# Kernel optimization log

Hardware: AMD Instinct MI355X
Metric: run time of the kernel (lower is better)

The kernel has to match this reference:

```python
import jax, jax.numpy as jnp
import numpy as np

B, T, HID = 16, 512, 1024
NH, NKV, D = 8, 4, 128
THETA = 10000.0


def setup_inputs() -> dict:
    key = jax.random.key(0)
    k0, k1, k2, k3, k4 = jax.random.split(key, 5)
    s = 0.02
    return {
        "hidden_states": jax.random.normal(k0, (B, T, HID), dtype=jnp.float32),
        "Wq": s * jax.random.normal(k1, (HID, NH * D), dtype=jnp.float32),
        "Wk": s * jax.random.normal(k2, (HID, NKV * D), dtype=jnp.float32),
        "Wv": s * jax.random.normal(k3, (HID, NKV * D), dtype=jnp.float32),
        "Wo": s * jax.random.normal(k4, (NH * D, HID), dtype=jnp.float32),
    }


def _rotate_half(x):
    x1, x2 = x[..., : x.shape[-1] // 2], x[..., x.shape[-1] // 2:]
    return jnp.concatenate((-x2, x1), axis=-1)


def reference(hidden_states, Wq, Wk, Wv, Wo):
    b, t, _ = hidden_states.shape
    # projections -> [B, H, T, D]
    q = (hidden_states @ Wq).reshape(b, t, NH, D).transpose(0, 2, 1, 3)
    k = (hidden_states @ Wk).reshape(b, t, NKV, D).transpose(0, 2, 1, 3)
    v = (hidden_states @ Wv).reshape(b, t, NKV, D).transpose(0, 2, 1, 3)

    # RoPE: cos/sin [T, D]
    inv_freq = 1.0 / (THETA ** (jnp.arange(0, D, 2, dtype=jnp.float32) / D))
    freqs = jnp.outer(jnp.arange(t, dtype=jnp.float32), inv_freq)
    emb = jnp.concatenate((freqs, freqs), axis=-1)
    cos, sin = jnp.cos(emb), jnp.sin(emb)
    q = q * cos + _rotate_half(q) * sin
    k = k * cos + _rotate_half(k) * sin

    # repeat_interleave KV heads to match query heads (GQA)
    groups = NH // NKV
    k = jnp.repeat(k, groups, axis=1)  # [B, NH, T, D]
    v = jnp.repeat(v, groups, axis=1)

    scale = 1.0 / jnp.sqrt(jnp.float32(D))
    attn = jnp.einsum("bhtd,bhsd->bhts", q, k) * scale  # [B, NH, T, T]
    causal = jnp.triu(jnp.ones((t, t), dtype=bool), k=1)
    attn = jnp.where(causal, -jnp.inf, attn)
    attn = jax.nn.softmax(attn, axis=-1)  # dropout p=0 (eval)

    out = jnp.einsum("bhts,bhsd->bhtd", attn, v)
    out = out.transpose(0, 2, 1, 3).reshape(b, t, NH * D)
    return out @ Wo  # [B, T, HID]
```

## Files before the change

kernel.cpp:

```cpp
#include <hip/hip_runtime.h>
#include <hip/hip_bf16.h>
#include <math.h>

#define Bn 16
#define Tn 512
#define HIDn 1024
#define NHn 8
#define NKVn 4
#define Dn 128

typedef __attribute__((ext_vector_type(8))) short short8;
typedef __attribute__((ext_vector_type(4))) float floatx4;

__device__ __forceinline__ short bf16r(float f) {
  __hip_bfloat16 h = __float2bfloat16(f);
  return *(short*)&h;
}
__device__ __forceinline__ float bf16f(short s) {
  __hip_bfloat16 h = *(__hip_bfloat16*)&s;
  return __bfloat162float(h);
}

__device__ __forceinline__ void g2l16(const short* g, short* l) {
  __builtin_amdgcn_global_load_lds(
      (const __attribute__((address_space(1))) void*)g,
      (__attribute__((address_space(3))) void*)l, 16, 0, 0);
}

__global__ __launch_bounds__(256) void prep_kernel(const float* __restrict__ X,
                                                   const float* __restrict__ Wq,
                                                   const float* __restrict__ Wk,
                                                   const float* __restrict__ Wv,
                                                   const float* __restrict__ Wo,
                                                   short* __restrict__ Xb,
                                                   short* __restrict__ BtQKV,
                                                   short* __restrict__ Wot) {
  __shared__ float tile[32][33];
  int bid = blockIdx.x;
  if (bid < 4096) {
    int i = bid * 256 + threadIdx.x;
    const float4* p = reinterpret_cast<const float4*>(X) + (size_t)i * 2;
    float4 a = p[0], b = p[1];
    short8 o;
    o[0] = bf16r(a.x); o[1] = bf16r(a.y); o[2] = bf16r(a.z); o[3] = bf16r(a.w);
    o[4] = bf16r(b.x); o[5] = bf16r(b.y); o[6] = bf16r(b.z); o[7] = bf16r(b.w);
    reinterpret_cast<short8*>(Xb)[i] = o;
    return;
  }
  int t = bid - 4096;
  const float* in;
  short* out;
  int N;
  if (t < 1024)      { in = Wq; out = BtQKV;               N = 1024; }
  else if (t < 1536) { t -= 1024; in = Wk; out = BtQKV + 1024 * 1024; N = 512; }
  else if (t < 2048) { t -= 1536; in = Wv; out = BtQKV + 1536 * 1024; N = 512; }
  else               { t -= 2048; in = Wo; out = Wot;                N = 1024; }
  int ntx = N >> 5;
  int n0 = (t % ntx) * 32, k0 = (t / ntx) * 32;
  int tx = threadIdx.x & 31, ty = threadIdx.x >> 5;
  for (int i = 0; i < 32; i += 8)
    tile[ty + i][tx] = in[(size_t)(k0 + ty + i) * N + n0 + tx];
  __syncthreads();
  for (int i = 0; i < 32; i += 8)
    out[(size_t)(n0 + ty + i) * 1024 + k0 + tx] = bf16r(tile[tx][ty + i]);
}

__global__ __launch_bounds__(512, 2) void gemm_qkv(const short* __restrict__ A,
                                                   const short* __restrict__ Bt,
                                                   short* __restrict__ Cqkv,
                                                   short* __restrict__ Vt) {
  __shared__ __align__(16) short SH[65536];
  const int tid = threadIdx.x;
  const int wave = tid >> 6, lane = tid & 63;
  const int quad = lane >> 4, l16 = lane & 15;
  const int wr = wave >> 2, wc = wave & 3;
  int fid = blockIdx.y * 8 + blockIdx.x;
  int swz = (fid & 7) * 32 + (fid >> 3);
  const int bx = swz & 7;
  const int m0 = (swz >> 3) << 8, n0 = bx << 8;
  const int nt = 16;

  floatx4 acc[2][2][4][2];
#pragma unroll
  for (int r = 0; r < 2; ++r)
#pragma unroll
    for (int c = 0; c < 2; ++c)
#pragma unroll
      for (int mi = 0; mi < 4; ++mi)
#pragma unroll
        for (int ni = 0; ni < 2; ++ni)
          acc[r][c][mi][ni] = (floatx4){0.f, 0.f, 0.f, 0.f};

  const int srow = tid >> 3;
  const int schunk = (tid & 7) ^ (srow & 7);

#define STAGE(tile_, src_, row0_, ldso_)                                             \
  do {                                                                               \
    int t_ = (tile_);                                                                \
    if (t_ < nt) {                                                                   \
      short* bb_ = SH + ((t_ & 1) << 15) + (ldso_);                                  \
      const short* sp_ =                                                             \
          (src_) + ((size_t)((row0_) + srow) << 10) + (t_ << 6) + (schunk << 3);     \
      g2l16(sp_, bb_ + (wave << 9));                                                 \
      g2l16(sp_ + (64 << 10), bb_ + 4096 + (wave << 9));                             \
    }                                                                                \
  } while (0)

#define LDA(dst_, rhalf_)                                                            \
  do {                                                                               \
    _Pragma("unroll") for (int mi = 0; mi < 4; ++mi) {                               \
      int R = (rhalf_) * 128 + wr * 64 + mi * 16 + l16;                              \
      _Pragma("unroll") for (int k = 0; k < 2; ++k) {                                \
        int pos = (k * 4 + quad) ^ (R & 7);                                          \
        dst_[mi][k] = *(const short8*)&Ab[R * 64 + pos * 8];                         \
      }                                                                              \
    }                                                                                \
  } while (0)

#define LDB(dst_, chalf_)                                                            \
  do {                                                                               \
    _Pragma("unroll") for (int ni = 0; ni < 2; ++ni) {                               \
      int R = (chalf_) * 128 + wc * 32 + ni * 16 + l16;                              \
      _Pragma("unroll") for (int k = 0; k < 2; ++k) {                                \
        int pos = (k * 4 + quad) ^ (R & 7);                                          \
        dst_[ni][k] = *(const short8*)&Bb[R * 64 + pos * 8];                         \
      }                                                                              \
    }                                                                                \
  } while (0)

#define MFMA_Q(r_, c_, a_, b_)                                                       \
  do {                                                                               \
    _Pragma("unroll") for (int mi = 0; mi < 4; ++mi)                                 \
        _Pragma("unroll") for (int ni = 0; ni < 2; ++ni) {                           \
      acc[r_][c_][mi][ni] = __builtin_amdgcn_mfma_f32_16x16x32_bf16(                 \
          a_[mi][0], b_[ni][0], acc[r_][c_][mi][ni], 0, 0, 0);                       \
      acc[r_][c_][mi][ni] = __builtin_amdgcn_mfma_f32_16x16x32_bf16(                 \
          a_[mi][1], b_[ni][1], acc[r_][c_][mi][ni], 0, 0, 0);                       \
    }                                                                                \
  } while (0)

#define PH_OPEN()                                                                    \
  do {                                                                               \
    __builtin_amdgcn_s_barrier();                                                    \
    __builtin_amdgcn_s_setprio(1);                                                   \
  } while (0)
#define PH_CLOSE()                                                                   \
  do {                                                                               \
    __builtin_amdgcn_s_setprio(0);                                                   \
    __builtin_amdgcn_s_barrier();                                                    \
  } while (0)

  STAGE(0, A, m0, 0);
  STAGE(0, Bt, n0 + 128, 24576);
  STAGE(0, Bt, n0, 16384);
  STAGE(0, A, m0 + 128, 8192);
  STAGE(1, A, m0, 0);
  STAGE(1, Bt, n0 + 128, 24576);
  STAGE(1, Bt, n0, 16384);
  asm volatile("s_waitcnt vmcnt(6)" ::: "memory");
  __builtin_amdgcn_s_barrier();

  short8 afA[4][2], afB[4][2], bf0[2][2], bf1[2][2];
  for (int g = 0; g < nt; ++g) {
    const short* Ab = SH + ((g & 1) << 15);
    const short* Bb = Ab + 16384;
    LDA(afA, 0);
    LDB(bf0, 0);
    LDB(bf1, 1);
    STAGE(g + 1, A, m0 + 128, 8192);
    PH_OPEN();
    MFMA_Q(0, 0, afA, bf0);
    PH_CLOSE();
    LDA(afB, 1);
    STAGE(g + 2, A, m0, 0);
    PH_OPEN();
    MFMA_Q(0, 1, afA, bf1);
    PH_CLOSE();
    STAGE(g + 2, Bt, n0 + 128, 24576);
    PH_OPEN();
    MFMA_Q(1, 1, afB, bf1);
    PH_CLOSE();
    STAGE(g + 2, Bt, n0, 16384);
    PH_OPEN();
    MFMA_Q(1, 0, afB, bf0);
    __builtin_amdgcn_s_setprio(0);
    if (g + 2 < nt)
      asm volatile("s_waitcnt vmcnt(6)" ::: "memory");
    else
      asm volatile("s_waitcnt vmcnt(0)" ::: "memory");
    __builtin_amdgcn_s_barrier();
  }

  if (bx < 6) {
#pragma unroll
    for (int r = 0; r < 2; ++r)
#pragma unroll
      for (int c = 0; c < 2; ++c)
#pragma unroll
        for (int mi = 0; mi < 4; ++mi)
#pragma unroll
          for (int ni = 0; ni < 2; ++ni)
#pragma unroll
            for (int rr = 0; rr < 4; ++rr) {
              int row = m0 + r * 128 + wr * 64 + mi * 16 + quad * 4 + rr;
              int col = n0 + c * 128 + wc * 32 + ni * 16 + l16;
              Cqkv[(size_t)row * 2048 + col] = bf16r(acc[r][c][mi][ni][rr]);
            }
  } else {
    const int b = m0 >> 9, t0 = m0 & (Tn - 1);
#pragma unroll
    for (int ch = 0; ch < 2; ++ch) {
      __syncthreads();
#pragma unroll
      for (int r = 0; r < 2; ++r)
#pragma unroll
        for (int mi = 0; mi < 4; ++mi)
#pragma unroll
          for (int ni = 0; ni < 2; ++ni)
#pragma unroll
            for (int rr = 0; rr < 4; ++rr) {
              int t = r * 128 + wr * 64 + mi * 16 + quad * 4 + rr;
              int d = wc * 32 + ni * 16 + l16;
              SH[d * 264 + t] = bf16r(acc[r][ch][mi][ni][rr]);
            }
      __syncthreads();
      int kv = (bx - 6) * 2 + ch;
#pragma unroll
      for (int u = 0; u < 8; ++u) {
        int idx = tid + u * 512;
        int d = idx >> 5, tb = (idx & 31) << 3;
        short8 vv = *(short8*)&SH[d * 264 + tb];
        *(short8*)&Vt[((size_t)(b * NKVn + kv) * 128 + d) * Tn + t0 + tb] = vv;
      }
    }
  }
#undef STAGE
#undef LDA
#undef LDB
#undef MFMA_Q
#undef PH_OPEN
#undef PH_CLOSE
}

__global__ void rope_k_kernel(short* __restrict__ C) {
  int idx = blockIdx.x * blockDim.x + threadIdx.x;
  int vec = idx & 7;
  int head = (idx >> 3) & 3;
  int bt = idx >> 5;
  int t = bt & (Tn - 1);
  int i0 = vec * 8;
  size_t base = (size_t)bt * 2048 + 1024 + head * 128 + i0;
  short8 x1 = *(short8*)&C[base];
  short8 x2 = *(short8*)&C[base + 64];
  short8 o1, o2;
  float tf = (float)t;
#pragma unroll
  for (int j = 0; j < 8; ++j) {
    float a = tf * exp2f(-0.2076205059f * (float)(i0 + j));
    float s, c;
    sincosf(a, &s, &c);
    float v1 = bf16f(x1[j]), v2 = bf16f(x2[j]);
    o1[j] = bf16r(v1 * c - v2 * s);
    o2[j] = bf16r(v2 * c + v1 * s);
  }
  *(short8*)&C[base] = o1;
  *(short8*)&C[base + 64] = o2;
}

__global__ __launch_bounds__(512, 2) void gemm_out(const short* __restrict__ A,
                                                   const short* __restrict__ Bt,
                                                   float* __restrict__ Cout) {
  __shared__ __align__(16) short SH[49152];
  const int tid = threadIdx.x;
  const int wave = tid >> 6, lane = tid & 63;
  const int quad = lane >> 4, l16 = lane & 15;
  const int wr = wave >> 2, wc = wave & 3;
  int fid = blockIdx.y * 8 + blockIdx.x;
  int swz = (fid & 7) * 32 + (fid >> 3);
  const int m0 = (swz >> 3) << 8;
  const int n0 = (swz & 7) << 7;
  const int nt = 16;

  floatx4 acc[2][4][2];
#pragma unroll
  for (int r = 0; r < 2; ++r)
#pragma unroll
    for (int mi = 0; mi < 4; ++mi)
#pragma unroll
      for (int ni = 0; ni < 2; ++ni)
        acc[r][mi][ni] = (floatx4){0.f, 0.f, 0.f, 0.f};

  const int srow = tid >> 3;
  const int schunk = (tid & 7) ^ (srow & 7);

#define STAGE(tile_, src_, row0_, ldso_)                                             \
  do {                                                                               \
    int t_ = (tile_);                                                                \
    if (t_ < nt) {                                                                   \
      short* bb_ = SH + (t_ & 1) * 24576 + (ldso_);                                  \
      const short* sp_ =                                                             \
          (src_) + ((size_t)((row0_) + srow) << 10) + (t_ << 6) + (schunk << 3);     \
      g2l16(sp_, bb_ + (wave << 9));                                                 \
      g2l16(sp_ + (64 << 10), bb_ + 4096 + (wave << 9));                             \
    }                                                                                \
  } while (0)

#define LDA(dst_, rhalf_)                                                            \
  do {                                                                               \
    _Pragma("unroll") for (int mi = 0; mi < 4; ++mi) {                               \
      int R = (rhalf_) * 128 + wr * 64 + mi * 16 + l16;                              \
      _Pragma("unroll") for (int k = 0; k < 2; ++k) {                                \
        int pos = (k * 4 + quad) ^ (R & 7);                                          \
        dst_[mi][k] = *(const short8*)&Ab[R * 64 + pos * 8];                         \
      }                                                                              \
    }                                                                                \
  } while (0)

#define LDB()                                                                        \
  do {                                                                               \
    _Pragma("unroll") for (int ni = 0; ni < 2; ++ni) {                               \
      int R = wc * 32 + ni * 16 + l16;                                               \
      _Pragma("unroll") for (int k = 0; k < 2; ++k) {                                \
        int pos = (k * 4 + quad) ^ (R & 7);                                          \
        bf0[ni][k] = *(const short8*)&Bb[R * 64 + pos * 8];                          \
      }                                                                              \
    }                                                                                \
  } while (0)

#define MFMA_Q(r_, a_)                                                               \
  do {                                                                               \
    _Pragma("unroll") for (int mi = 0; mi < 4; ++mi)                                 \
        _Pragma("unroll") for (int ni = 0; ni < 2; ++ni) {                           \
      acc[r_][mi][ni] = __builtin_amdgcn_mfma_f32_16x16x32_bf16(                     \
          a_[mi][0], bf0[ni][0], acc[r_][mi][ni], 0, 0, 0);                          \
      acc[r_][mi][ni] = __builtin_amdgcn_mfma_f32_16x16x32_bf16(                     \
          a_[mi][1], bf0[ni][1], acc[r_][mi][ni], 0, 0, 0);                          \
    }                                                                                \
  } while (0)

#define PH_OPEN()                                                                    \
  do {                                                                               \
    __builtin_amdgcn_s_barrier();                                                    \
    __builtin_amdgcn_s_setprio(1);                                                   \
  } while (0)
#define PH_CLOSE()                                                                   \
  do {                                                                               \
    __builtin_amdgcn_s_setprio(0);                                                   \
    __builtin_amdgcn_s_barrier();                                                    \
  } while (0)

  STAGE(0, A, m0, 0);
  STAGE(0, Bt, n0, 16384);
  STAGE(0, A, m0 + 128, 8192);
  STAGE(1, A, m0, 0);
  STAGE(1, Bt, n0, 16384);
  asm volatile("s_waitcnt vmcnt(4)" ::: "memory");
  __builtin_amdgcn_s_barrier();

  short8 afA[4][2], afB[4][2], bf0[2][2];
  for (int g = 0; g < nt; ++g) {
    const short* Ab = SH + (g & 1) * 24576;
    const short* Bb = Ab + 16384;
    LDA(afA, 0);
    LDB();
    LDA(afB, 1);
    STAGE(g + 1, A, m0 + 128, 8192);
    PH_OPEN();
    MFMA_Q(0, afA);
    PH_CLOSE();
    STAGE(g + 2, A, m0, 0);
    STAGE(g + 2, Bt, n0, 16384);
    PH_OPEN();
    MFMA_Q(1, afB);
    __builtin_amdgcn_s_setprio(0);
    if (g + 2 < nt)
      asm volatile("s_waitcnt vmcnt(4)" ::: "memory");
    else
      asm volatile("s_waitcnt vmcnt(0)" ::: "memory");
    __builtin_amdgcn_s_barrier();
  }

#pragma unroll
  for (int r = 0; r < 2; ++r)
#pragma unroll
    for (int mi = 0; mi < 4; ++mi)
#pragma unroll
      for (int ni = 0; ni < 2; ++ni)
#pragma unroll
        for (int rr = 0; rr < 4; ++rr) {
          int row = m0 + r * 128 + wr * 64 + mi * 16 + quad * 4 + rr;
          int col = n0 + wc * 32 + ni * 16 + l16;
          Cout[(size_t)row * 1024 + col] = acc[r][mi][ni][rr];
        }
#undef STAGE
#undef LDA
#undef LDB
#undef MFMA_Q
#undef PH_OPEN
#undef PH_CLOSE
}

__global__ __launch_bounds__(256) void attn_kernel(const short* __restrict__ Cqkv,
                                                   const short* __restrict__ Vt,
                                                   short* __restrict__ Aout) {
  __shared__ __align__(16) short SH[20992];
  short* Ks = SH;
  short (*Ps)[16][72] = reinterpret_cast<short(*)[16][72]>(SH + 16384);
  const int tid = threadIdx.x;
  const int wave = tid >> 6, lane = tid & 63;
  const int quad = lane >> 4, l16 = lane & 15;
  const int blk = blockIdx.x;
  const int qt = 7 - (blk >> 7);
  const int h = blk & 7, b = (blk >> 3) & 15;
  const int kvh = h >> 1;
  const short* Qp = Cqkv + (size_t)b * Tn * 2048 + h * 128;
  const short* Kp = Cqkv + (size_t)b * Tn * 2048 + 1024 + kvh * 128;
  const short* Vtp = Vt + (size_t)(b * NKVn + kvh) * 128 * Tn;

  const int qrow0 = qt * 64 + wave * 16;
  const float scale = 0.12753378904f;

#define STAGEK(k0_, b_)                                                       \
  do {                                                                        \
    _Pragma("unroll") for (int v = 0; v < 4; ++v) {                           \
      int s_ = tid + v * 256;                                                 \
      int r_ = s_ >> 4, c_ = (s_ & 15) ^ (r_ & 15);                           \
      g2l16(&Kp[(size_t)((k0_) + r_) * 2048 + c_ * 8],                        \
            Ks + ((b_) << 13) + (v * 256 + wave * 64) * 8);                   \
    }                                                                         \
  } while (0)

  short8 qf[4];
#pragma unroll
  for (int kc = 0; kc < 4; ++kc)
    qf[kc] = *(const short8*)&Qp[(size_t)(qrow0 + l16) * 2048 + kc * 32 + quad * 8];

  STAGEK(0, 0);

  {
    float tf = (float)(qrow0 + l16);
#pragma unroll
    for (int kc = 0; kc < 2; ++kc)
#pragma unroll
      for (int j = 0; j < 8; ++j) {
        int d = kc * 32 + quad * 8 + j;
        float a = tf * exp2f(-0.2076205059f * (float)d);
        float s, c;
        sincosf(a, &s, &c);
        float x1 = bf16f(qf[kc][j]), x2 = bf16f(qf[kc + 2][j]);
        qf[kc][j] = bf16r((x1 * c - x2 * s) * scale);
        qf[kc + 2][j] = bf16r((x2 * c + x1 * s) * scale);
      }
  }

  floatx4 o[8];
  float l_part[4];
#pragma unroll
  for (int ni = 0; ni < 8; ++ni) o[ni] = (floatx4){0.f, 0.f, 0.f, 0.f};
#pragma unroll
  for (int r = 0; r < 4; ++r) l_part[r] = 0.f;

  const int ntiles = qt + 1;
  __syncthreads();

  for (int it = 0; it < ntiles; ++it) {
    const int k0 = it << 6;
    const short* Kb = Ks + ((it & 1) << 13);

    short8 vf0[8], vf1[8];
#pragma unroll
    for (int ni = 0; ni < 8; ++ni) {
      const short* vp = &Vtp[(size_t)(ni * 16 + l16) * Tn + k0 + quad * 8];
      vf0[ni] = *(const short8*)vp;
      vf1[ni] = *(const short8*)(vp + 32);
    }

    if (it + 1 < ntiles) STAGEK(k0 + 64, (it + 1) & 1);

    floatx4 s[4];
    __builtin_amdgcn_s_setprio(1);
#pragma unroll
    for (int ni = 0; ni < 4; ++ni) {
      s[ni] = (floatx4){0.f, 0.f, 0.f, 0.f};
      short8 kf[4];
#pragma unroll
      for (int kc = 0; kc < 4; ++kc) {
        int R = ni * 16 + l16;
        int pos = (kc * 4 + quad) ^ (R & 15);
        kf[kc] = *(short8*)&Kb[R * 128 + pos * 8];
      }
#pragma unroll
      for (int kc = 0; kc < 4; ++kc)
        s[ni] = __builtin_amdgcn_mfma_f32_16x16x32_bf16(qf[kc], kf[kc], s[ni], 0, 0, 0);
    }
    __builtin_amdgcn_s_setprio(0);

    const bool diag = (k0 + 63 > qrow0);
#pragma unroll
    for (int ni = 0; ni < 4; ++ni)
#pragma unroll
      for (int r = 0; r < 4; ++r) {
        float p = exp2f(s[ni][r]);
        if (diag) {
          int key = k0 + ni * 16 + l16;
          int qr = qrow0 + quad * 4 + r;
          if (key > qr) p = 0.f;
        }
        s[ni][r] = p;
        l_part[r] += p;
      }

#pragma unroll
    for (int ni = 0; ni < 4; ++ni)
#pragma unroll
      for (int r = 0; r < 4; ++r)
        Ps[wave][quad * 4 + r][ni * 16 + l16] = bf16r(s[ni][r]);

    short8 pf[2];
#pragma unroll
    for (int kc = 0; kc < 2; ++kc)
      pf[kc] = *(short8*)&Ps[wave][l16][kc * 32 + quad * 8];
    __builtin_amdgcn_s_setprio(1);
#pragma unroll
    for (int ni = 0; ni < 8; ++ni) {
      o[ni] = __builtin_amdgcn_mfma_f32_16x16x32_bf16(pf[0], vf0[ni], o[ni], 0, 0, 0);
      o[ni] = __builtin_amdgcn_mfma_f32_16x16x32_bf16(pf[1], vf1[ni], o[ni], 0, 0, 0);
    }
    __builtin_amdgcn_s_setprio(0);

    if (it + 1 < ntiles) __syncthreads();
  }
#undef STAGEK

  float inv[4];
#pragma unroll
  for (int r = 0; r < 4; ++r) {
    float rs = l_part[r];
#pragma unroll
    for (int off = 8; off >= 1; off >>= 1) rs += __shfl_xor(rs, off, 16);
    inv[r] = 1.0f / rs;
  }
#pragma unroll
  for (int ni = 0; ni < 8; ++ni)
#pragma unroll
    for (int r = 0; r < 4; ++r) {
      int t = qrow0 + quad * 4 + r;
      int d = ni * 16 + l16;
      Aout[((size_t)b * Tn + t) * 1024 + h * 128 + d] = bf16r(o[ni][r] * inv[r]);
    }
}

extern "C" void kernel_launch(void* const* d_in, const int* in_sizes, int n_in,
                              void* d_out, int out_size, void* d_ws, size_t ws_size,
                              hipStream_t stream) {
  const float* X  = (const float*)d_in[0];
  const float* Wq = (const float*)d_in[1];
  const float* Wk = (const float*)d_in[2];
  const float* Wv = (const float*)d_in[3];
  const float* Wo = (const float*)d_in[4];

  char* ws = (char*)d_ws;
  short* Xb    = (short*)(ws);
  short* BtQKV = (short*)(ws + (16ull << 20));
  short* Wot   = (short*)(ws + (20ull << 20));
  short* Cqkv  = (short*)(ws + (22ull << 20));
  short* Vt    = (short*)(ws + (54ull << 20));
  short* Aout  = (short*)(ws + (62ull << 20));

  prep_kernel<<<7168, 256, 0, stream>>>(X, Wq, Wk, Wv, Wo, Xb, BtQKV, Wot);
  gemm_qkv<<<dim3(8, 32), 512, 0, stream>>>(Xb, BtQKV, Cqkv, Vt);
  rope_k_kernel<<<1024, 256, 0, stream>>>(Cqkv);
  attn_kernel<<<1024, 256, 0, stream>>>(Cqkv, Vt, Aout);
  gemm_out<<<dim3(8, 32), 512, 0, stream>>>(Aout, Wot, (float*)d_out);
}
```

Measured before the change: 203.5 us.

## Split attention into single-wave blocks loading K directly into registers

The attention kernel changes from 256-thread blocks, where four waves share double-buffered K tiles in LDS, to 64-thread single-wave blocks (4096 blocks). Each wave now loads its K fragments straight from global memory into registers and prefetches the next tile while running the PV MFMAs. This removes the block-wide __syncthreads and LDS staging. In exchange, K tiles are no longer shared across waves, which raises global/L2 traffic, and register use goes up.

```diff
diff --git a/kernel.cpp b/kernel.cpp
--- a/kernel.cpp
+++ b/kernel.cpp
@@ -400,42 +400,34 @@
 #undef PH_CLOSE
 }
 
-__global__ __launch_bounds__(256) void attn_kernel(const short* __restrict__ Cqkv,
-                                                   const short* __restrict__ Vt,
-                                                   short* __restrict__ Aout) {
-  __shared__ __align__(16) short SH[20992];
-  short* Ks = SH;
-  short (*Ps)[16][72] = reinterpret_cast<short(*)[16][72]>(SH + 16384);
-  const int tid = threadIdx.x;
-  const int wave = tid >> 6, lane = tid & 63;
+__global__ __launch_bounds__(64) void attn_kernel(const short* __restrict__ Cqkv,
+                                                  const short* __restrict__ Vt,
+                                                  short* __restrict__ Aout) {
+  __shared__ short Ps[16][72];
+  const int lane = threadIdx.x;
   const int quad = lane >> 4, l16 = lane & 15;
   const int blk = blockIdx.x;
-  const int qt = 7 - (blk >> 7);
-  const int h = blk & 7, b = (blk >> 3) & 15;
+  const int qt = 7 - (blk >> 9);
+  const int h = blk & 7, b = (blk >> 3) & 15, ws = (blk >> 7) & 3;
   const int kvh = h >> 1;
   const short* Qp = Cqkv + (size_t)b * Tn * 2048 + h * 128;
   const short* Kp = Cqkv + (size_t)b * Tn * 2048 + 1024 + kvh * 128;
   const short* Vtp = Vt + (size_t)(b * NKVn + kvh) * 128 * Tn;
 
-  const int qrow0 = qt * 64 + wave * 16;
+  const int qrow0 = qt * 64 + ws * 16;
   const float scale = 0.12753378904f;
-
-#define STAGEK(k0_, b_)                                                       \
-  do {                                                                        \
-    _Pragma("unroll") for (int v = 0; v < 4; ++v) {                           \
-      int s_ = tid + v * 256;                                                 \
-      int r_ = s_ >> 4, c_ = (s_ & 15) ^ (r_ & 15);                           \
-      g2l16(&Kp[(size_t)((k0_) + r_) * 2048 + c_ * 8],                        \
-            Ks + ((b_) << 13) + (v * 256 + wave * 64) * 8);                   \
-    }                                                                         \
-  } while (0)
 
   short8 qf[4];
 #pragma unroll
   for (int kc = 0; kc < 4; ++kc)
     qf[kc] = *(const short8*)&Qp[(size_t)(qrow0 + l16) * 2048 + kc * 32 + quad * 8];
 
-  STAGEK(0, 0);
+  short8 kf[4][4];
+#pragma unroll
+  for (int ni = 0; ni < 4; ++ni)
+#pragma unroll
+    for (int kc = 0; kc < 4; ++kc)
+      kf[ni][kc] = *(const short8*)&Kp[(size_t)(ni * 16 + l16) * 2048 + kc * 32 + quad * 8];
 
   {
     float tf = (float)(qrow0 + l16);
@@ -461,11 +453,20 @@
   for (int r = 0; r < 4; ++r) l_part[r] = 0.f;
 
   const int ntiles = qt + 1;
-  __syncthreads();
 
   for (int it = 0; it < ntiles; ++it) {
     const int k0 = it << 6;
-    const short* Kb = Ks + ((it & 1) << 13);
+
+    floatx4 s[4];
+    __builtin_amdgcn_s_setprio(1);
+#pragma unroll
+    for (int ni = 0; ni < 4; ++ni) {
+      s[ni] = (floatx4){0.f, 0.f, 0.f, 0.f};
+#pragma unroll
+      for (int kc = 0; kc < 4; ++kc)
+        s[ni] = __builtin_amdgcn_mfma_f32_16x16x32_bf16(qf[kc], kf[ni][kc], s[ni], 0, 0, 0);
+    }
+    __builtin_amdgcn_s_setprio(0);
 
     short8 vf0[8], vf1[8];
 #pragma unroll
@@ -474,26 +475,6 @@
       vf0[ni] = *(const short8*)vp;
       vf1[ni] = *(const short8*)(vp + 32);
     }
-
-    if (it + 1 < ntiles) STAGEK(k0 + 64, (it + 1) & 1);
-
-    floatx4 s[4];
-    __builtin_amdgcn_s_setprio(1);
-#pragma unroll
-    for (int ni = 0; ni < 4; ++ni) {
-      s[ni] = (floatx4){0.f, 0.f, 0.f, 0.f};
-      short8 kf[4];
-#pragma unroll
-      for (int kc = 0; kc < 4; ++kc) {
-        int R = ni * 16 + l16;
-        int pos = (kc * 4 + quad) ^ (R & 15);
-        kf[kc] = *(short8*)&Kb[R * 128 + pos * 8];
-      }
-#pragma unroll
-      for (int kc = 0; kc < 4; ++kc)
-        s[ni] = __builtin_amdgcn_mfma_f32_16x16x32_bf16(qf[kc], kf[kc], s[ni], 0, 0, 0);
-    }
-    __builtin_amdgcn_s_setprio(0);
 
     const bool diag = (k0 + 63 > qrow0);
 #pragma unroll
@@ -514,12 +495,22 @@
     for (int ni = 0; ni < 4; ++ni)
 #pragma unroll
       for (int r = 0; r < 4; ++r)
-        Ps[wave][quad * 4 + r][ni * 16 + l16] = bf16r(s[ni][r]);
+        Ps[quad * 4 + r][ni * 16 + l16] = bf16r(s[ni][r]);
 
     short8 pf[2];
 #pragma unroll
     for (int kc = 0; kc < 2; ++kc)
-      pf[kc] = *(short8*)&Ps[wave][l16][kc * 32 + quad * 8];
+      pf[kc] = *(short8*)&Ps[l16][kc * 32 + quad * 8];
+
+    if (it + 1 < ntiles) {
+      const short* kp = Kp + (size_t)(k0 + 64) * 2048;
+#pragma unroll
+      for (int ni = 0; ni < 4; ++ni)
+#pragma unroll
+        for (int kc = 0; kc < 4; ++kc)
+          kf[ni][kc] = *(const short8*)&kp[(size_t)(ni * 16 + l16) * 2048 + kc * 32 + quad * 8];
+    }
+
     __builtin_amdgcn_s_setprio(1);
 #pragma unroll
     for (int ni = 0; ni < 8; ++ni) {
@@ -527,10 +518,7 @@
       o[ni] = __builtin_amdgcn_mfma_f32_16x16x32_bf16(pf[1], vf1[ni], o[ni], 0, 0, 0);
     }
     __builtin_amdgcn_s_setprio(0);
-
-    if (it + 1 < ntiles) __syncthreads();
-  }
-#undef STAGEK
+  }
 
   float inv[4];
 #pragma unroll
@@ -570,6 +558,6 @@
   prep_kernel<<<7168, 256, 0, stream>>>(X, Wq, Wk, Wv, Wo, Xb, BtQKV, Wot);
   gemm_qkv<<<dim3(8, 32), 512, 0, stream>>>(Xb, BtQKV, Cqkv, Vt);
   rope_k_kernel<<<1024, 256, 0, stream>>>(Cqkv);
-  attn_kernel<<<1024, 256, 0, stream>>>(Cqkv, Vt, Aout);
+  attn_kernel<<<4096, 64, 0, stream>>>(Cqkv, Vt, Aout);
   gemm_out<<<dim3(8, 32), 512, 0, stream>>>(Aout, Wot, (float*)d_out);
 }
```

Result: slower. 223.3 us (+9.7%).
